# Performance work log

Hardware: AMD Instinct MI355X
Metric: run time of the kernel (lower is better)

Reference implementation:

```python
import jax, jax.numpy as jnp
import numpy as np

MIN_NORM = 1e-15
PROJ_EPS = 4e-3  # HGCN float32 boundary eps
C = 1.0          # curvature (all layers)
N_BRANCH = 4


def artanh(x):
    return jnp.arctanh(jnp.clip(x, -1.0 + 1e-7, 1.0 - 1e-7))


def _norm(x):
    return jnp.clip(jnp.linalg.norm(x, axis=-1, keepdims=True), MIN_NORM)


def proj(x, c):
    n = _norm(x)
    maxn = (1.0 - PROJ_EPS) / jnp.sqrt(c)
    return jnp.where(n > maxn, x / n * maxn, x)


def expmap0(u, c):
    sc = jnp.sqrt(c)
    n = _norm(u)
    return jnp.tanh(sc * n) * u / (sc * n)


def logmap0(p, c):
    sc = jnp.sqrt(c)
    n = _norm(p)
    return artanh(sc * n) * p / (sc * n)


def mobius_add(x, y, c):
    x2 = jnp.sum(x * x, -1, keepdims=True)
    y2 = jnp.sum(y * y, -1, keepdims=True)
    xy = jnp.sum(x * y, -1, keepdims=True)
    num = (1.0 + 2.0 * c * xy + c * y2) * x + (1.0 - c * x2) * y
    den = 1.0 + 2.0 * c * xy + c * c * x2 * y2
    return num / jnp.clip(den, MIN_NORM)


def mobius_matvec(W, x, c):
    sc = jnp.sqrt(c)
    xn = _norm(x)
    mx = x @ W.T
    mxn = _norm(mx)
    res = jnp.tanh(mxn / xn * artanh(sc * xn)) * mx / (mxn * sc)
    zero = jnp.all(mx == 0, axis=-1, keepdims=True)
    return jnp.where(zero, jnp.zeros((), x.dtype), res)


def mobius_mulscaler(r, x, c):
    sc = jnp.sqrt(c)
    xn = _norm(x)
    return jnp.tanh(r * artanh(sc * xn)) * x / (xn * sc)


def spmm(src, dst, w, xt, n):
    # out[i] = sum_{e: dst[e]=i} w[e] * xt[src[e]]
    return jax.ops.segment_sum(w[:, None] * xt[src], dst, num_segments=n)


def hgc_layer(h, W, b, src, dst, w, n):
    # HypLinear (dropout=0)
    h = proj(mobius_matvec(W, h, C), C)
    hb = proj(expmap0(b[None, :], C), C)
    h = proj(mobius_add(h, hb, C), C)
    # HypAgg: sparse propagation in tangent space
    st = spmm(src, dst, w, logmap0(h, C), n)
    h = proj(expmap0(st, C), C)
    # HypAct (relu)
    return proj(expmap0(jax.nn.relu(logmap0(h, C)), C), C)


def encode(x, W0, b0, W1, b1, src, dst, w, n):
    h = proj(expmap0(x, C), C)  # proj_tan0 is identity on Poincare ball
    h = hgc_layer(h, W0, b0, src, dst, w, n)
    h = hgc_layer(h, W1, b1, src, dst, w, n)
    return h


def setup_inputs() -> dict:
    key = jax.random.key(0)
    ks = jax.random.split(key, 8)
    N, F_IN, HID, DIM, E = 50000, 128, 128, 64, 1600000
    x = jax.random.normal(ks[0], (N, F_IN), jnp.float32)
    edge_src = jax.random.randint(ks[1], (E,), 0, N, jnp.int32)
    edge_dst = jax.random.randint(ks[2], (E,), 0, N, jnp.int32)
    # positive, roughly row-normalized edge weights (avg degree 32)
    edge_w = jax.random.uniform(ks[3], (N_BRANCH, E), jnp.float32) / 32.0
    W0 = jax.random.normal(ks[4], (N_BRANCH, HID, F_IN), jnp.float32) * 0.05
    b0 = jax.random.normal(ks[5], (N_BRANCH, HID), jnp.float32) * 0.01
    W1 = jax.random.normal(ks[6], (N_BRANCH, DIM, HID), jnp.float32) * 0.05
    b1 = jax.random.normal(ks[7], (N_BRANCH, DIM), jnp.float32) * 0.01
    return {"x": x, "edge_src": edge_src, "edge_dst": edge_dst, "edge_w": edge_w,
            "W0": W0, "b0": b0, "W1": W1, "b1": b1}


def reference(x, edge_src, edge_dst, edge_w, W0, b0, W1, b1):
    n = x.shape[0]
    # 4 directional-proximity branches (d_i, d_o, n_i, n_o); fixed small loop
    branches = [encode(x, W0[i], b0[i], W1[i], b1[i], edge_src, edge_dst, edge_w[i], n)
                for i in range(N_BRANCH)]
    # Mobius-weighted (scalar 1/8) combination, left-to-right mobius_add chain
    target = mobius_mulscaler(0.125, branches[0], C)
    for br in branches[1:]:
        target = mobius_add(target, mobius_mulscaler(0.125, br, C), C)
    feat = jnp.stack(branches + [target], axis=1)  # [N, 5, dim]
    # HypAttnAgg (use_att=False) with row-normalized per-node star adjacency:
    # target row of each 5-block = mean of the 5 tangent vectors
    agg = logmap0(feat, C).mean(axis=1)            # [N, dim]
    return proj(expmap0(agg, C), C)
```

## Files before the change

### kernel.cpp

```cpp
#include <hip/hip_runtime.h>
#include <math.h>

#define MAXN_P 0.996f

typedef unsigned short bfraw;
typedef __attribute__((ext_vector_type(8))) short bf16x8;
typedef __attribute__((ext_vector_type(4))) float f32x4;

__device__ __forceinline__ float wred(float v){
  #pragma unroll
  for(int o=32;o>0;o>>=1) v += __shfl_xor(v,o,64);
  return v;
}
template<int W>
__device__ __forceinline__ float gredw(float v){
  #pragma unroll
  for(int o=W/2;o>0;o>>=1) v += __shfl_xor(v,o,64);
  return v;
}
__device__ __forceinline__ float artanh_c(float x){
  x = fminf(fmaxf(x, -1.0f+1e-7f), 1.0f-1e-7f);
  return atanhf(x);
}
__device__ __forceinline__ float sel4(float4 w, int g){
  float ab = (g&1) ? w.y : w.x;
  float cd = (g&1) ? w.w : w.z;
  return (g&2) ? cd : ab;
}
__device__ __forceinline__ bfraw f2bf(float f){
  unsigned u = __float_as_uint(f);
  unsigned r = (u + 0x7fffu + ((u>>16)&1u)) >> 16;
  return (bfraw)r;
}
__device__ __forceinline__ float bflo(unsigned u){ return __uint_as_float(u<<16); }
__device__ __forceinline__ float bfhi(unsigned u){ return __uint_as_float(u & 0xffff0000u); }

__device__ __forceinline__ void acc8(float* a, float w, uint4 u){
  a[0]=fmaf(w, bflo(u.x), a[0]); a[1]=fmaf(w, bfhi(u.x), a[1]);
  a[2]=fmaf(w, bflo(u.y), a[2]); a[3]=fmaf(w, bfhi(u.y), a[3]);
  a[4]=fmaf(w, bflo(u.z), a[4]); a[5]=fmaf(w, bfhi(u.z), a[5]);
  a[6]=fmaf(w, bflo(u.w), a[6]); a[7]=fmaf(w, bfhi(u.w), a[7]);
}
__device__ __forceinline__ void acc4(float* a, float w, uint2 u){
  a[0]=fmaf(w, bflo(u.x), a[0]); a[1]=fmaf(w, bfhi(u.x), a[1]);
  a[2]=fmaf(w, bflo(u.y), a[2]); a[3]=fmaf(w, bfhi(u.y), a[3]);
}

template<int W, int K>
__device__ __forceinline__ float postK(const float* u, float* h){
  float ss = 0.f;
  #pragma unroll
  for(int k=0;k<K;k++) ss += u[k]*u[k];
  ss = gredw<W>(ss);
  float un = fmaxf(sqrtf(ss), 1e-15f);
  float t1 = tanhf(un);
  float sc = t1/un;
  float pn = t1;
  if (pn > MAXN_P){ sc *= MAXN_P/pn; pn = MAXN_P; }
  float ln = fmaxf(pn, 1e-15f);
  float m = sc * (artanh_c(ln)/ln);
  float v[K]; float vs = 0.f;
  #pragma unroll
  for(int k=0;k<K;k++){ v[k] = fmaxf(u[k]*m, 0.f); vs += v[k]*v[k]; }
  vs = gredw<W>(vs);
  float vn = fmaxf(sqrtf(vs), 1e-15f);
  float t2 = tanhf(vn);
  float qs = t2/vn;
  float qn = t2;
  if (qn > MAXN_P){ qs *= MAXN_P/qn; qn = MAXN_P; }
  #pragma unroll
  for(int k=0;k<K;k++) h[k] = v[k]*qs;
  return qn;
}

__global__ void k_hist(const int* __restrict__ dst, int* __restrict__ cnt, int E){
  int e = blockIdx.x*blockDim.x + threadIdx.x;
  if (e < E) atomicAdd(&cnt[dst[e]], 1);
}

__global__ void k_scan(const int* __restrict__ cnt, int* __restrict__ rowptr,
                       int* __restrict__ cursor, int N){
  __shared__ int sh[1024];
  int t = threadIdx.x;
  int chunk = (N + 1023) / 1024;
  int b = t*chunk;
  int e = b + chunk; if (e > N) e = N;
  int s = 0;
  for(int i=b;i<e && i<N;i++) s += cnt[i];
  sh[t] = s;
  __syncthreads();
  for(int off=1; off<1024; off<<=1){
    int add = (t>=off) ? sh[t-off] : 0;
    __syncthreads();
    sh[t] += add;
    __syncthreads();
  }
  int run = (t==0) ? 0 : sh[t-1];
  for(int i=b;i<e && i<N;i++){
    rowptr[i] = run; cursor[i] = run; run += cnt[i];
  }
  if (t == 1023) rowptr[N] = run;
}

__global__ void k_fill(const int* __restrict__ src, const int* __restrict__ dst,
                       const float* __restrict__ ew, int E,
                       int* __restrict__ cursor, int* __restrict__ srcs,
                       float4* __restrict__ wq){
  int e = blockIdx.x*blockDim.x + threadIdx.x;
  if (e >= E) return;
  int d = dst[e];
  int pos = atomicAdd(&cursor[d], 1);
  srcs[pos] = src[e];
  wq[pos] = make_float4(ew[e], ew[(size_t)E + e], ew[2*(size_t)E + e], ew[3*(size_t)E + e]);
}

__global__ void k_exp0(const float* __restrict__ x, bfraw* __restrict__ h0,
                       float* __restrict__ n0, int N){
  int wid = (blockIdx.x*blockDim.x + threadIdx.x)>>6;
  int lane = threadIdx.x & 63;
  if (wid >= N) return;
  const float* r = x + (size_t)wid*128;
  float u0 = r[lane], u1 = r[lane+64];
  float ss = wred(u0*u0 + u1*u1);
  float un = fmaxf(sqrtf(ss), 1e-15f);
  float tn = tanhf(un);
  float sc = tn/un;
  float pn = tn;
  if (pn > MAXN_P){ sc *= MAXN_P/pn; pn = MAXN_P; }
  h0[(size_t)wid*128 + lane]      = f2bf(u0*sc);
  h0[(size_t)wid*128 + lane + 64] = f2bf(u1*sc);
  if (lane == 0) n0[wid] = pn;
}

__global__ void k_hb(const float* __restrict__ b0, const float* __restrict__ b1,
                     float* __restrict__ hb0, float* __restrict__ hb1,
                     int HID, int DIM){
  int bl = blockIdx.x;
  int lane = threadIdx.x;
  int layer = bl >> 2, br = bl & 3;
  int D = layer ? DIM : HID;
  const float* b = layer ? (b1 + (size_t)br*DIM) : (b0 + (size_t)br*HID);
  float* o       = layer ? (hb1 + (size_t)br*DIM) : (hb0 + (size_t)br*HID);
  float v0 = (lane < D) ? b[lane] : 0.f;
  float v1 = (lane+64 < D) ? b[lane+64] : 0.f;
  float ss = wred(v0*v0 + v1*v1);
  float n = fmaxf(sqrtf(ss), 1e-15f);
  float tn = tanhf(n);
  float sc = tn/n;
  if (tn > MAXN_P) sc *= MAXN_P/tn;
  if (lane < D)    o[lane]    = v0*sc;
  if (lane+64 < D) o[lane+64] = v1*sc;
}

__global__ void k_w2bf(const float* __restrict__ a, bfraw* __restrict__ o, int n){
  int i = blockIdx.x*blockDim.x + threadIdx.x;
  if (i < n) o[i] = f2bf(a[i]);
}

template<int CT>
__global__ __launch_bounds__(256) void k_gemm_fused(
    const bfraw* __restrict__ Abase, int lda, int abroff,
    const bfraw* __restrict__ Wb,
    const float* __restrict__ nin, int nstride, int nbroff,
    const float* __restrict__ hball,
    bfraw* __restrict__ xt,
    int M)
{
  constexpr int BN = CT*16;
  __shared__ bfraw tile[64*BN];
  int br = blockIdx.z;
  const bfraw* A = Abase + (size_t)br*abroff;
  const bfraw* W = Wb + (size_t)br*BN*128;
  const float* hb = hball + (size_t)br*BN;
  int rb = blockIdx.x*64;
  int t = threadIdx.x;
  int wave = t>>6, lane = t&63;
  int cl = lane&15, grp = lane>>4;

  int rowA = rb + wave*16 + cl;
  bf16x8 afr[4];
  bf16x8 zf = {0,0,0,0,0,0,0,0};
  #pragma unroll
  for(int ks=0;ks<4;ks++){
    if (rowA < M) afr[ks] = *(const bf16x8*)(A + (size_t)rowA*lda + ks*32 + grp*8);
    else          afr[ks] = zf;
  }
  f32x4 acc[CT];
  #pragma unroll
  for(int ct=0;ct<CT;ct++) acc[ct] = f32x4{0.f,0.f,0.f,0.f};
  #pragma unroll
  for(int ct=0;ct<CT;ct++){
    #pragma unroll
    for(int ks=0;ks<4;ks++){
      bf16x8 bfr = *(const bf16x8*)(W + (size_t)(ct*16+cl)*128 + ks*32 + grp*8);
      acc[ct] = __builtin_amdgcn_mfma_f32_16x16x32_bf16(afr[ks], bfr, acc[ct], 0,0,0);
    }
  }
  float hv[CT]; float hb2 = 0.f;
  #pragma unroll
  for(int ct=0;ct<CT;ct++){ hv[ct] = hb[cl+16*ct]; hb2 += hv[ct]*hv[ct]; }
  hb2 = gredw<16>(hb2);
  #pragma unroll
  for(int j=0;j<4;j++){
    int rloc = wave*16 + grp*4 + j;
    int node = rb + rloc;
    bool v = node < M;
    float m[CT]; float ss = 0.f;
    #pragma unroll
    for(int ct=0;ct<CT;ct++){ m[ct] = acc[ct][j]; ss += m[ct]*m[ct]; }
    ss = gredw<16>(ss);
    float mxn_raw = sqrtf(ss);
    float mxn = fmaxf(mxn_raw, 1e-15f);
    float xn = fmaxf(v ? nin[(size_t)node*nstride + br*nbroff] : 1.f, 1e-15f);
    float th = tanhf(mxn/xn * artanh_c(xn));
    float hs = (mxn_raw > 0.f) ? th/mxn : 0.f;
    float hn = (mxn_raw > 0.f) ? th : 0.f;
    if (hn > MAXN_P){ hs *= MAXN_P/hn; hn = MAXN_P; }
    float h[CT]; float xy = 0.f, x2 = 0.f;
    #pragma unroll
    for(int ct=0;ct<CT;ct++){ h[ct] = m[ct]*hs; xy += h[ct]*hv[ct]; x2 += h[ct]*h[ct]; }
    xy = gredw<16>(xy); x2 = gredw<16>(x2);
    float c1 = 1.f + 2.f*xy + hb2;
    float c2 = 1.f - x2;
    float den = fmaxf(1.f + 2.f*xy + x2*hb2, 1e-15f);
    float a[CT]; float as = 0.f;
    #pragma unroll
    for(int ct=0;ct<CT;ct++){ a[ct] = (c1*h[ct] + c2*hv[ct])/den; as += a[ct]*a[ct]; }
    as = gredw<16>(as);
    float an = fmaxf(sqrtf(as), 1e-15f);
    float s2 = 1.f;
    if (an > MAXN_P){ s2 = MAXN_P/an; an = MAXN_P; }
    float ls = artanh_c(an)/an * s2;
    #pragma unroll
    for(int ct=0;ct<CT;ct++) tile[rloc*BN + cl + 16*ct] = f2bf(a[ct]*ls);
  }
  __syncthreads();
  constexpr int IT = (64*BN)/(256*8);
  #pragma unroll
  for(int i=0;i<IT;i++){
    int flat = (t + i*256)*8;
    int row = flat/BN, col = flat%BN;
    int node = rb + row;
    if (node < M)
      *(uint4*)(xt + ((size_t)node*4 + br)*BN + col) = *(const uint4*)(tile + row*BN + col);
  }
}

__global__ __launch_bounds__(256) void k_spmm_l0(const int* __restrict__ rowptr,
                        const int* __restrict__ srcs, const float4* __restrict__ wq,
                        const bfraw* __restrict__ xt,
                        bfraw* __restrict__ hout, float* __restrict__ n4, int N){
  int wid = (blockIdx.x*blockDim.x + threadIdx.x)>>6;
  int lane = threadIdx.x & 63;
  if (wid >= N) return;
  int g = lane>>4;
  float acc[8] = {0,0,0,0,0,0,0,0};
  int p0 = rowptr[wid], p1 = rowptr[wid+1];
  int p = p0;
  for (; p+8 <= p1; p += 8){
    int s[8]; float4 w[8]; uint4 u[8];
    #pragma unroll
    for(int i=0;i<8;i++){ s[i] = srcs[p+i]; w[i] = wq[p+i]; }
    #pragma unroll
    for(int i=0;i<8;i++) u[i] = *((const uint4*)(xt + (size_t)s[i]*512) + lane);
    #pragma unroll
    for(int i=0;i<8;i++) acc8(acc, sel4(w[i],g), u[i]);
  }
  for (; p+2 <= p1; p += 2){
    int s0 = srcs[p], s1 = srcs[p+1];
    float4 w0 = wq[p], w1 = wq[p+1];
    uint4 u0 = *((const uint4*)(xt + (size_t)s0*512) + lane);
    uint4 u1 = *((const uint4*)(xt + (size_t)s1*512) + lane);
    acc8(acc, sel4(w0,g), u0);
    acc8(acc, sel4(w1,g), u1);
  }
  if (p < p1){
    int s0 = srcs[p];
    float4 w0 = wq[p];
    uint4 u0 = *((const uint4*)(xt + (size_t)s0*512) + lane);
    acc8(acc, sel4(w0,g), u0);
  }
  float h[8];
  float qn = postK<16,8>(acc, h);
  uint4 o;
  o.x = (unsigned)f2bf(h[0]) | ((unsigned)f2bf(h[1])<<16);
  o.y = (unsigned)f2bf(h[2]) | ((unsigned)f2bf(h[3])<<16);
  o.z = (unsigned)f2bf(h[4]) | ((unsigned)f2bf(h[5])<<16);
  o.w = (unsigned)f2bf(h[6]) | ((unsigned)f2bf(h[7])<<16);
  *((uint4*)(hout + (size_t)wid*512) + lane) = o;
  if ((lane&15)==0) n4[(size_t)wid*4 + g] = qn;
}

__global__ __launch_bounds__(256) void k_spmm_l1(const int* __restrict__ rowptr,
                        const int* __restrict__ srcs, const float4* __restrict__ wq,
                        const bfraw* __restrict__ xt,
                        float* __restrict__ out, int N){
  int wid = (blockIdx.x*blockDim.x + threadIdx.x)>>6;
  int lane = threadIdx.x & 63;
  if (wid >= N) return;
  int g = lane>>4;
  int slot = lane & 15;
  float acc[4] = {0,0,0,0};
  int p0 = rowptr[wid], p1 = rowptr[wid+1];
  int p = p0;
  for (; p+8 <= p1; p += 8){
    int s[8]; float4 w[8]; uint2 u[8];
    #pragma unroll
    for(int i=0;i<8;i++){ s[i] = srcs[p+i]; w[i] = wq[p+i]; }
    #pragma unroll
    for(int i=0;i<8;i++) u[i] = *((const uint2*)(xt + (size_t)s[i]*256) + lane);
    #pragma unroll
    for(int i=0;i<8;i++) acc4(acc, sel4(w[i],g), u[i]);
  }
  for (; p+2 <= p1; p += 2){
    int s0 = srcs[p], s1 = srcs[p+1];
    float4 w0 = wq[p], w1 = wq[p+1];
    uint2 u0 = *((const uint2*)(xt + (size_t)s0*256) + lane);
    uint2 u1 = *((const uint2*)(xt + (size_t)s1*256) + lane);
    acc4(acc, sel4(w0,g), u0);
    acc4(acc, sel4(w1,g), u1);
  }
  if (p < p1){
    int s0 = srcs[p];
    float4 w0 = wq[p];
    uint2 u0 = *((const uint2*)(xt + (size_t)s0*256) + lane);
    acc4(acc, sel4(w0,g), u0);
  }
  float hv[4];
  float qn = postK<16,4>(acc, hv);
  float xk[4][4]; float qk[4];
  #pragma unroll
  for(int k=0;k<4;k++){
    #pragma unroll
    for(int j=0;j<4;j++) xk[k][j] = __shfl(hv[j], slot + 16*k, 64);
    qk[k] = __shfl(qn, 16*k, 64);
  }
  float xn0 = fmaxf(qk[0], 1e-15f);
  float s0 = tanhf(0.125f*artanh_c(xn0))/xn0;
  float t[4] = {s0*xk[0][0], s0*xk[0][1], s0*xk[0][2], s0*xk[0][3]};
  #pragma unroll
  for(int k=1;k<4;k++){
    float yn = fmaxf(qk[k], 1e-15f);
    float sy = tanhf(0.125f*artanh_c(yn))/yn;
    float y[4] = {sy*xk[k][0], sy*xk[k][1], sy*xk[k][2], sy*xk[k][3]};
    float dx=0.f, dy=0.f, dxy=0.f;
    #pragma unroll
    for(int j=0;j<4;j++){ dx += t[j]*t[j]; dy += y[j]*y[j]; dxy += t[j]*y[j]; }
    float x2 = gredw<16>(dx);
    float y2 = gredw<16>(dy);
    float xy = gredw<16>(dxy);
    float c1 = 1.f + 2.f*xy + y2;
    float c2 = 1.f - x2;
    float den = fmaxf(1.f + 2.f*xy + x2*y2, 1e-15f);
    #pragma unroll
    for(int j=0;j<4;j++) t[j] = (c1*t[j] + c2*y[j])/den;
  }
  float s[4] = {0,0,0,0};
  #pragma unroll
  for(int k=0;k<4;k++){
    float nk = fmaxf(qk[k], 1e-15f);
    float lk = artanh_c(nk)/nk;
    #pragma unroll
    for(int j=0;j<4;j++) s[j] = fmaf(lk, xk[k][j], s[j]);
  }
  float dt = 0.f;
  #pragma unroll
  for(int j=0;j<4;j++) dt += t[j]*t[j];
  float tn = fmaxf(sqrtf(gredw<16>(dt)), 1e-15f);
  float lt = artanh_c(tn)/tn;
  #pragma unroll
  for(int j=0;j<4;j++) s[j] = 0.2f*fmaf(lt, t[j], s[j]);
  float ds = 0.f;
  #pragma unroll
  for(int j=0;j<4;j++) ds += s[j]*s[j];
  float an = fmaxf(sqrtf(gredw<16>(ds)), 1e-15f);
  float on = tanhf(an);
  float osc = on/an;
  if (on > MAXN_P) osc *= MAXN_P/on;
  if (g == 0)
    *(float4*)(out + (size_t)wid*64 + 4*slot) =
      make_float4(s[0]*osc, s[1]*osc, s[2]*osc, s[3]*osc);
}

extern "C" void kernel_launch(void* const* d_in, const int* in_sizes, int n_in,
                              void* d_out, int out_size, void* d_ws, size_t ws_size,
                              hipStream_t stream){
  const float* x   = (const float*)d_in[0];
  const int*   src = (const int*)d_in[1];
  const int*   dst = (const int*)d_in[2];
  const float* ew  = (const float*)d_in[3];
  const float* W0  = (const float*)d_in[4];
  const float* b0  = (const float*)d_in[5];
  const float* W1  = (const float*)d_in[6];
  const float* b1  = (const float*)d_in[7];
  float* out = (float*)d_out;

  const int FIN = 128;
  int N = in_sizes[0]/FIN;
  int E = in_sizes[1];
  int HID = in_sizes[5]/4;
  int DIM = in_sizes[7]/4;

  char* ws = (char*)d_ws;
  size_t off = 0;
  auto alloc = [&](size_t bytes)->char*{
    char* p = ws + off;
    off += (bytes + 255) & ~(size_t)255;
    return p;
  };
  bfraw* h4b    = (bfraw*)alloc((size_t)N*4*FIN*2);
  bfraw* xtb    = (bfraw*)alloc((size_t)N*4*FIN*2);
  float* n0     = (float*)alloc((size_t)N*4);
  float* n4     = (float*)alloc((size_t)N*16);
  int*   rowptr = (int*)alloc((size_t)(N+1)*4);
  int*   cnt    = (int*)alloc((size_t)N*4);
  int*   cursor = (int*)alloc((size_t)N*4);
  int*   srcs   = (int*)alloc((size_t)E*4);
  float4* wq    = (float4*)alloc((size_t)E*16);
  float* hb0    = (float*)alloc((size_t)4*HID*4);
  float* hb1    = (float*)alloc((size_t)4*DIM*4);
  bfraw* w0b    = (bfraw*)alloc((size_t)4*HID*FIN*2);
  bfraw* w1b    = (bfraw*)alloc((size_t)4*DIM*HID*2);
  (void)ws_size; (void)n_in; (void)out_size;

  bfraw* h0 = h4b;

  int rowBlocks  = (N + 3)/4;

  hipMemsetAsync(cnt, 0, (size_t)N*4, stream);
  k_hist<<<(E+255)/256, 256, 0, stream>>>(dst, cnt, E);
  k_scan<<<1, 1024, 0, stream>>>(cnt, rowptr, cursor, N);
  k_fill<<<(E+255)/256, 256, 0, stream>>>(src, dst, ew, E, cursor, srcs, wq);

  k_exp0<<<rowBlocks, 256, 0, stream>>>(x, h0, n0, N);
  k_hb<<<8, 64, 0, stream>>>(b0, b1, hb0, hb1, HID, DIM);
  k_w2bf<<<(4*HID*FIN+255)/256, 256, 0, stream>>>(W0, w0b, 4*HID*FIN);
  k_w2bf<<<(4*DIM*HID+255)/256, 256, 0, stream>>>(W1, w1b, 4*DIM*HID);

  k_gemm_fused<8><<<dim3((N+63)/64, 1, 4), 256, 0, stream>>>(
      h0, FIN, 0, w0b, n0, 1, 0, hb0, xtb, N);
  k_spmm_l0<<<rowBlocks, 256, 0, stream>>>(rowptr, srcs, wq, xtb, h4b, n4, N);

  k_gemm_fused<4><<<dim3((N+63)/64, 1, 4), 256, 0, stream>>>(
      h4b, 4*HID, HID, w1b, n4, 4, 1, hb1, xtb, N);
  k_spmm_l1<<<rowBlocks, 256, 0, stream>>>(rowptr, srcs, wq, xtb, out, N);
}
```

Measured before the change: 804.5 us.

## Merge prologue kernels into one launch and parallelize CSR row-pointer scan

Folds the histogram, expmap0 of the inputs, weight conversion to bf16 and bias expmap into a single block-partitioned prologue kernel, cutting four launches to one and letting the independent pieces overlap on the device. It also replaces the single-block 1024-thread serial-chunk scan with a three-phase multi-block scan (block sums, serial prefix over block sums, local scan). This removes launch gaps and the slow single-block scan, but adds two small kernels, and the middle phase is a single-thread loop.

```diff
diff --git a/kernel.cpp b/kernel.cpp
--- a/kernel.cpp
+++ b/kernel.cpp
@@ -73,33 +73,124 @@
   return qn;
 }
 
-__global__ void k_hist(const int* __restrict__ dst, int* __restrict__ cnt, int E){
-  int e = blockIdx.x*blockDim.x + threadIdx.x;
-  if (e < E) atomicAdd(&cnt[dst[e]], 1);
-}
-
-__global__ void k_scan(const int* __restrict__ cnt, int* __restrict__ rowptr,
-                       int* __restrict__ cursor, int N){
-  __shared__ int sh[1024];
-  int t = threadIdx.x;
-  int chunk = (N + 1023) / 1024;
-  int b = t*chunk;
-  int e = b + chunk; if (e > N) e = N;
-  int s = 0;
-  for(int i=b;i<e && i<N;i++) s += cnt[i];
-  sh[t] = s;
+__global__ __launch_bounds__(256) void k_prologue(
+    const float* __restrict__ x, bfraw* __restrict__ h0, float* __restrict__ n0, int N,
+    const int* __restrict__ dst, int* __restrict__ cnt, int E,
+    const float* __restrict__ W0, bfraw* __restrict__ w0b, int nW0,
+    const float* __restrict__ W1, bfraw* __restrict__ w1b, int nW1,
+    const float* __restrict__ b0, const float* __restrict__ b1,
+    float* __restrict__ hb0, float* __restrict__ hb1, int HID, int DIM,
+    int RB, int HIST, int W0B, int W1B)
+{
+  int b = blockIdx.x;
+  int tid = threadIdx.x;
+  if (b < RB){
+    int wid = (b*256 + tid)>>6;
+    int lane = tid & 63;
+    if (wid >= N) return;
+    const float* r = x + (size_t)wid*128;
+    float u0 = r[lane], u1 = r[lane+64];
+    float ss = wred(u0*u0 + u1*u1);
+    float un = fmaxf(sqrtf(ss), 1e-15f);
+    float tn = tanhf(un);
+    float sc = tn/un;
+    float pn = tn;
+    if (pn > MAXN_P){ sc *= MAXN_P/pn; pn = MAXN_P; }
+    h0[(size_t)wid*128 + lane]      = f2bf(u0*sc);
+    h0[(size_t)wid*128 + lane + 64] = f2bf(u1*sc);
+    if (lane == 0) n0[wid] = pn;
+    return;
+  }
+  b -= RB;
+  if (b < HIST){
+    int e = b*256 + tid;
+    if (e < E) atomicAdd(&cnt[dst[e]], 1);
+    return;
+  }
+  b -= HIST;
+  if (b < W0B){
+    int i = b*256 + tid;
+    if (i < nW0) w0b[i] = f2bf(W0[i]);
+    return;
+  }
+  b -= W0B;
+  if (b < W1B){
+    int i = b*256 + tid;
+    if (i < nW1) w1b[i] = f2bf(W1[i]);
+    return;
+  }
+  b -= W1B;
+  {
+    if (tid >= 64) return;
+    int layer = b >> 2, br = b & 3;
+    int D = layer ? DIM : HID;
+    const float* bb = layer ? (b1 + (size_t)br*DIM) : (b0 + (size_t)br*HID);
+    float* o        = layer ? (hb1 + (size_t)br*DIM) : (hb0 + (size_t)br*HID);
+    float v0 = (tid < D) ? bb[tid] : 0.f;
+    float v1 = (tid+64 < D) ? bb[tid+64] : 0.f;
+    float ss = wred(v0*v0 + v1*v1);
+    float n = fmaxf(sqrtf(ss), 1e-15f);
+    float tn = tanhf(n);
+    float sc = tn/n;
+    if (tn > MAXN_P) sc *= MAXN_P/tn;
+    if (tid < D)    o[tid]    = v0*sc;
+    if (tid+64 < D) o[tid+64] = v1*sc;
+  }
+}
+
+__global__ __launch_bounds__(256) void k_scan1(const int* __restrict__ cnt, int* __restrict__ bsum, int N){
+  __shared__ int sh[256];
+  int base = blockIdx.x*2048;
+  int tid = threadIdx.x;
+  int loc = 0;
+  #pragma unroll
+  for(int j=0;j<8;j++){
+    int i = base + tid*8 + j;
+    loc += (i < N) ? cnt[i] : 0;
+  }
+  sh[tid] = loc;
   __syncthreads();
-  for(int off=1; off<1024; off<<=1){
-    int add = (t>=off) ? sh[t-off] : 0;
+  for(int off=128; off>0; off>>=1){
+    if (tid < off) sh[tid] += sh[tid+off];
     __syncthreads();
-    sh[t] += add;
+  }
+  if (tid == 0) bsum[blockIdx.x] = sh[0];
+}
+__global__ void k_scan2(int* __restrict__ bsum, int nb){
+  if (threadIdx.x == 0){
+    int run = 0;
+    for(int i=0;i<nb;i++){ int t = bsum[i]; bsum[i] = run; run += t; }
+  }
+}
+__global__ __launch_bounds__(256) void k_scan3(const int* __restrict__ cnt, const int* __restrict__ bsum,
+                                               int* __restrict__ rowptr, int* __restrict__ cursor, int N){
+  __shared__ int sh[256];
+  int base = blockIdx.x*2048;
+  int tid = threadIdx.x;
+  int v[8]; int loc = 0;
+  #pragma unroll
+  for(int j=0;j<8;j++){
+    int i = base + tid*8 + j;
+    v[j] = (i < N) ? cnt[i] : 0;
+    loc += v[j];
+  }
+  sh[tid] = loc;
+  __syncthreads();
+  for(int off=1; off<256; off<<=1){
+    int add = (tid>=off) ? sh[tid-off] : 0;
     __syncthreads();
-  }
-  int run = (t==0) ? 0 : sh[t-1];
-  for(int i=b;i<e && i<N;i++){
-    rowptr[i] = run; cursor[i] = run; run += cnt[i];
-  }
-  if (t == 1023) rowptr[N] = run;
+    sh[tid] += add;
+    __syncthreads();
+  }
+  int run = ((tid==0) ? 0 : sh[tid-1]) + bsum[blockIdx.x];
+  #pragma unroll
+  for(int j=0;j<8;j++){
+    int i = base + tid*8 + j;
+    if (i < N){
+      rowptr[i] = run; cursor[i] = run; run += v[j];
+      if (i == N-1) rowptr[N] = run;
+    }
+  }
 }
 
 __global__ void k_fill(const int* __restrict__ src, const int* __restrict__ dst,
@@ -112,49 +203,6 @@
   int pos = atomicAdd(&cursor[d], 1);
   srcs[pos] = src[e];
   wq[pos] = make_float4(ew[e], ew[(size_t)E + e], ew[2*(size_t)E + e], ew[3*(size_t)E + e]);
-}
-
-__global__ void k_exp0(const float* __restrict__ x, bfraw* __restrict__ h0,
-                       float* __restrict__ n0, int N){
-  int wid = (blockIdx.x*blockDim.x + threadIdx.x)>>6;
-  int lane = threadIdx.x & 63;
-  if (wid >= N) return;
-  const float* r = x + (size_t)wid*128;
-  float u0 = r[lane], u1 = r[lane+64];
-  float ss = wred(u0*u0 + u1*u1);
-  float un = fmaxf(sqrtf(ss), 1e-15f);
-  float tn = tanhf(un);
-  float sc = tn/un;
-  float pn = tn;
-  if (pn > MAXN_P){ sc *= MAXN_P/pn; pn = MAXN_P; }
-  h0[(size_t)wid*128 + lane]      = f2bf(u0*sc);
-  h0[(size_t)wid*128 + lane + 64] = f2bf(u1*sc);
-  if (lane == 0) n0[wid] = pn;
-}
-
-__global__ void k_hb(const float* __restrict__ b0, const float* __restrict__ b1,
-                     float* __restrict__ hb0, float* __restrict__ hb1,
-                     int HID, int DIM){
-  int bl = blockIdx.x;
-  int lane = threadIdx.x;
-  int layer = bl >> 2, br = bl & 3;
-  int D = layer ? DIM : HID;
-  const float* b = layer ? (b1 + (size_t)br*DIM) : (b0 + (size_t)br*HID);
-  float* o       = layer ? (hb1 + (size_t)br*DIM) : (hb0 + (size_t)br*HID);
-  float v0 = (lane < D) ? b[lane] : 0.f;
-  float v1 = (lane+64 < D) ? b[lane+64] : 0.f;
-  float ss = wred(v0*v0 + v1*v1);
-  float n = fmaxf(sqrtf(ss), 1e-15f);
-  float tn = tanhf(n);
-  float sc = tn/n;
-  if (tn > MAXN_P) sc *= MAXN_P/tn;
-  if (lane < D)    o[lane]    = v0*sc;
-  if (lane+64 < D) o[lane+64] = v1*sc;
-}
-
-__global__ void k_w2bf(const float* __restrict__ a, bfraw* __restrict__ o, int n){
-  int i = blockIdx.x*blockDim.x + threadIdx.x;
-  if (i < n) o[i] = f2bf(a[i]);
 }
 
 template<int CT>
@@ -421,21 +469,28 @@
   float* hb1    = (float*)alloc((size_t)4*DIM*4);
   bfraw* w0b    = (bfraw*)alloc((size_t)4*HID*FIN*2);
   bfraw* w1b    = (bfraw*)alloc((size_t)4*DIM*HID*2);
+  int*   bsum   = (int*)alloc((size_t)256*4);
   (void)ws_size; (void)n_in; (void)out_size;
 
   bfraw* h0 = h4b;
 
-  int rowBlocks  = (N + 3)/4;
+  int rowBlocks = (N + 3)/4;
+  int nW0 = 4*HID*FIN, nW1 = 4*DIM*HID;
+  int RB = rowBlocks;
+  int HIST = (E + 255)/256;
+  int W0B = (nW0 + 255)/256;
+  int W1B = (nW1 + 255)/256;
+  int nscan = (N + 2047)/2048;
 
   hipMemsetAsync(cnt, 0, (size_t)N*4, stream);
-  k_hist<<<(E+255)/256, 256, 0, stream>>>(dst, cnt, E);
-  k_scan<<<1, 1024, 0, stream>>>(cnt, rowptr, cursor, N);
-  k_fill<<<(E+255)/256, 256, 0, stream>>>(src, dst, ew, E, cursor, srcs, wq);
-
-  k_exp0<<<rowBlocks, 256, 0, stream>>>(x, h0, n0, N);
-  k_hb<<<8, 64, 0, stream>>>(b0, b1, hb0, hb1, HID, DIM);
-  k_w2bf<<<(4*HID*FIN+255)/256, 256, 0, stream>>>(W0, w0b, 4*HID*FIN);
-  k_w2bf<<<(4*DIM*HID+255)/256, 256, 0, stream>>>(W1, w1b, 4*DIM*HID);
+  k_prologue<<<RB + HIST + W0B + W1B + 8, 256, 0, stream>>>(
+      x, h0, n0, N, dst, cnt, E, W0, w0b, nW0, W1, w1b, nW1,
+      b0, b1, hb0, hb1, HID, DIM, RB, HIST, W0B, W1B);
+
+  k_scan1<<<nscan, 256, 0, stream>>>(cnt, bsum, N);
+  k_scan2<<<1, 64, 0, stream>>>(bsum, nscan);
+  k_scan3<<<nscan, 256, 0, stream>>>(cnt, bsum, rowptr, cursor, N);
+  k_fill<<<HIST, 256, 0, stream>>>(src, dst, ew, E, cursor, srcs, wq);
 
   k_gemm_fused<8><<<dim3((N+63)/64, 1, 4), 256, 0, stream>>>(
       h0, FIN, 0, w0b, n0, 1, 0, hb0, xtb, N);
```

After: 716.4 us. 10.9% less time.
